# Kernel tuning notes

Hardware: AMD Instinct MI355X
Metric: run time of the kernel (lower is better)

The kernel has to match this reference:

```python
import jax, jax.numpy as jnp
import numpy as np

N = 8192
IN_CH = 256
OUT_CH = 256


def setup_inputs() -> dict:
    key = jax.random.key(0)
    k1, k2, k3, k4, k5 = jax.random.split(key, 5)
    features = jax.random.normal(k1, (N, IN_CH), dtype=jnp.float32)
    wavelets = jax.random.normal(k2, (N, N), dtype=jnp.float32)
    wavelets_inv = jax.random.normal(k3, (N, N), dtype=jnp.float32)
    # parameters
    # xavier uniform for weight_matrix
    limit = np.sqrt(6.0 / (IN_CH + OUT_CH)).astype(np.float32)
    weight_matrix = jax.random.uniform(k4, (IN_CH, OUT_CH), minval=-limit, maxval=limit, dtype=jnp.float32)
    filt = jax.random.uniform(k5, (N,), minval=0.9, maxval=1.1, dtype=jnp.float32)
    return {"features": features, "wavelets": wavelets, "wavelets_inv": wavelets_inv,
            "weight_matrix": weight_matrix, "filt": filt}


def reference(features, wavelets, wavelets_inv, weight_matrix, filt):
    # transformed = features @ W                    [N, out]
    transformed = features @ weight_matrix
    # spectral = wavelets_inv @ transformed         [N, out]
    spectral = wavelets_inv @ transformed
    # torch.diag(filter) @ spectral == filt[:, None] * spectral (avoid NxN diag GEMM)
    filtered = filt[:, None] * spectral
    # output = wavelets @ filtered                  [N, out]
    return wavelets @ filtered
```

## Files before the change

### kernel.cpp

```cpp
#include <hip/hip_runtime.h>
#include <hip/hip_bf16.h>
#include <stdint.h>
#include <stddef.h>

typedef __bf16 bf16;
typedef float f32x4 __attribute__((ext_vector_type(4)));
typedef bf16 bf16x8 __attribute__((ext_vector_type(8)));
typedef bf16 bf16x4 __attribute__((ext_vector_type(4)));

#define MROWS 8192
#define NOUT 256
#define BK 128
#define NTHREADS 512
#define LDS_SMALL (32 * BK * 2)

#define SCHED0 __builtin_amdgcn_sched_barrier(0)
#define SBAR __builtin_amdgcn_s_barrier()


__global__ __launch_bounds__(NTHREADS, 1) void gemm_ks(
    const float* __restrict__ A, const bf16* __restrict__ Bp,
    float* __restrict__ wsP, float* __restrict__ doutP,
    const int kshift, const int nsteps, const int lda) {
  __shared__ char lds[2][32768];
  const int t = threadIdx.x;
  const int w = t >> 6;
  const int l = t & 63;
  const int ks = blockIdx.x & ((1 << kshift) - 1);
  const int mt = blockIdx.x >> kshift;
  const int m0 = mt * 128;
  const int ts0 = ks * nsteps;
  float* __restrict__ Ps =
      (ks == ((1 << kshift) - 1)) ? doutP : wsP + (size_t)ks * 2097152;

  const float* gAr[4];
#pragma unroll
  for (int j = 0; j < 4; ++j)
    gAr[j] = A + (size_t)(m0 + w * 16 + j * 2 + (l >> 5)) * (size_t)lda +
             (size_t)ts0 * BK + (l & 31) * 4;

  int awoff[8];
#pragma unroll
  for (int q = 0; q < 8; ++q) {
    const int r = w * 16 + q * 2 + (l >> 5);
    awoff[q] = r * 256 + ((((l & 31) * 8)) ^ ((r & 7) << 4));
  }

  int aoffb[4];
#pragma unroll
  for (int ak = 0; ak < 4; ++ak)
    aoffb[ak] = (l & 15) * 256 +
                ((ak * 64 + (l >> 4) * 16) ^ ((l & 7) << 4));

  const char* pBw = (const char*)Bp + w * 8192 + l * 16;

  f32x4 acc[8][2] = {};
  f32x4 pA[8];
  bf16x8 Ba[2][4], Bb[2][4];

#define LOAD_PA(KA)                                                           \
  {                                                                           \
    _Pragma("unroll") for (int j = 0; j < 4; ++j) {                           \
      pA[2 * j] = __builtin_nontemporal_load((const f32x4*)(gAr[j] + (KA)));  \
      pA[2 * j + 1] = __builtin_nontemporal_load(                             \
          (const f32x4*)(gAr[j] + (size_t)2 * lda * 4 / 4 * 0 + 0) + 0);      \
    }                                                                         \
  }
#undef LOAD_PA
  const float* gAq[8];
#pragma unroll
  for (int q = 0; q < 8; ++q)
    gAq[q] = A + (size_t)(m0 + w * 16 + q * 2 + (l >> 5)) * (size_t)lda +
             (size_t)ts0 * BK + (l & 31) * 4;

#pragma unroll
  for (int q = 0; q < 8; ++q)
    pA[q] = __builtin_nontemporal_load((const f32x4*)gAq[q]);
  SCHED0;
#pragma unroll
  for (int bfi = 0; bfi < 2; ++bfi)
#pragma unroll
    for (int ak = 0; ak < 4; ++ak)
      Ba[bfi][ak] = *(const bf16x8*)(pBw + ((size_t)ts0 << 16) +
                                     (bfi * 4 + ak) * 1024);
  SCHED0;
#pragma unroll
  for (int q = 0; q < 8; ++q) {
    bf16x4 pk;
#pragma unroll
    for (int e = 0; e < 4; ++e) pk[e] = (bf16)pA[q][e];
    *(bf16x4*)(lds[0] + awoff[q]) = pk;
  }
  SCHED0;
  {
    const int s1 = (nsteps > 1) ? BK : 0;
#pragma unroll
    for (int q = 0; q < 8; ++q)
      pA[q] = __builtin_nontemporal_load((const f32x4*)(gAq[q] + s1));
  }
  asm volatile("s_waitcnt lgkmcnt(0)" ::: "memory");
  SBAR;
  SCHED0;

#define BODY_K(S, PAR, BCUR, BNXT)                                            \
  {                                                                           \
    const char* rslot = lds[PAR];                                             \
    char* wslot = lds[PAR ^ 1];                                               \
    _Pragma("unroll") for (int q = 0; q < 8; ++q) {                           \
      bf16x4 pk;                                                              \
      _Pragma("unroll") for (int e = 0; e < 4; ++e) pk[e] = (bf16)pA[q][e];   \
      *(bf16x4*)(wslot + awoff[q]) = pk;                                      \
    }                                                                         \
    SCHED0;                                                                   \
    {                                                                         \
      const int tn = ((S) + 1 < nsteps) ? ts0 + (S) + 1 : ts0;                \
      _Pragma("unroll") for (int bfi = 0; bfi < 2; ++bfi)                     \
          _Pragma("unroll") for (int ak = 0; ak < 4; ++ak)                    \
              BNXT[bfi][ak] = *(const bf16x8*)(                               \
                  pBw + ((size_t)tn << 16) + (bfi * 4 + ak) * 1024);          \
    }                                                                         \
    SCHED0;                                                                   \
    {                                                                         \
      const int ka = ((S) + 2 < nsteps) ? ((S) + 2) * BK : 0;                 \
      _Pragma("unroll") for (int q = 0; q < 8; ++q)                           \
          pA[q] = __builtin_nontemporal_load((const f32x4*)(gAq[q] + ka));    \
    }                                                                         \
    SCHED0;                                                                   \
    __builtin_amdgcn_s_setprio(1);                                            \
    _Pragma("unroll") for (int ak = 0; ak < 4; ++ak) {                        \
      bf16x8 afr[8];                                                          \
      _Pragma("unroll") for (int af = 0; af < 8; ++af)                        \
          afr[af] = *(const bf16x8*)(rslot + af * 4096 + aoffb[ak]);          \
      _Pragma("unroll") for (int af = 0; af < 8; ++af)                        \
          _Pragma("unroll") for (int bfi = 0; bfi < 2; ++bfi)                 \
              acc[af][bfi] = __builtin_amdgcn_mfma_f32_16x16x32_bf16(         \
                  afr[af], BCUR[bfi][ak], acc[af][bfi], 0, 0, 0);             \
    }                                                                         \
    __builtin_amdgcn_s_setprio(0);                                            \
    SCHED0;                                                                   \
    asm volatile("s_waitcnt lgkmcnt(0)" ::: "memory");                        \
    SBAR;                                                                     \
    SCHED0;                                                                   \
  }

  for (int s = 0; s < nsteps; s += 2) {
    BODY_K(s, 0, Ba, Bb);
    BODY_K(s + 1, 1, Bb, Ba);
  }
#undef BODY_K

#pragma unroll
  for (int af = 0; af < 8; ++af)
#pragma unroll
    for (int bfi = 0; bfi < 2; ++bfi) {
      const int mb = m0 + af * 16 + (l >> 4) * 4;
      const int n = w * 32 + bfi * 16 + (l & 15);
#pragma unroll
      for (int j = 0; j < 4; ++j)
        Ps[(size_t)(mb + j) * NOUT + n] = acc[af][bfi][j];
    }
}

__global__ void reduce2(const float* __restrict__ wsP,
                        const float* __restrict__ doutP,
                        const float* __restrict__ filt, bf16* __restrict__ Fp,
                        const int KS) {
  const int n = threadIdx.x;
  const int m8 = blockIdx.x;
  bf16x8 pk;
#pragma unroll
  for (int r = 0; r < 8; ++r) {
    const int m = m8 * 8 + r;
    float s = doutP[(size_t)m * NOUT + n];
    for (int ks = 0; ks < KS - 1; ++ks)
      s += wsP[(size_t)ks * 2097152 + (size_t)m * NOUT + n];
    pk[r] = (bf16)(s * filt[m]);
  }
  const int ts = m8 >> 4, wq = n >> 5, bq = (n >> 4) & 1, aq = (m8 >> 2) & 3;
  const int lq = (m8 & 3) * 16 + (n & 15);
  *(bf16x8*)((char*)Fp +
             (size_t)(((ts * 64 + wq * 8 + bq * 4 + aq) << 10) + lq * 16)) = pk;
}

__global__ void reduce3(const float* __restrict__ wsP, float* __restrict__ doutP,
                        const int KS) {
  const size_t i = (size_t)blockIdx.x * 256 + threadIdx.x;
  float s = doutP[i];
  for (int ks = 0; ks < KS - 1; ++ks) s += wsP[(size_t)ks * 2097152 + i];
  doutP[i] = s;
}

template <bool SCALE, bool OUTT>
__global__ __launch_bounds__(NTHREADS, 1) void gemm_small(
    const float* __restrict__ A, const bf16* __restrict__ Bp,
    const float* __restrict__ filt, void* __restrict__ outp,
    const int K, const int lda) {
  __shared__ char lds[2][LDS_SMALL];
  const int t = threadIdx.x;
  const int w = t >> 6;
  const int l = t & 63;
  const int m0 = blockIdx.x * 32;
  const int NT = K / BK;

  const int ar = t >> 4;
  const int acb = t & 15;
  const float* gA = A + (size_t)(m0 + ar) * (size_t)lda + acb * 8;
  const int a_lds_off = (ar * (BK * 2) + acb * 16) ^ ((ar & 7) << 4);

  int aoff[2][4];
#pragma unroll
  for (int af = 0; af < 2; ++af)
#pragma unroll
    for (int ak = 0; ak < 4; ++ak) {
      const int r = af * 16 + (l & 15);
      const int kb = ak * 64 + (l >> 4) * 16;
      aoff[af][ak] = (r * (BK * 2) + kb) ^ ((r & 7) << 4);
    }

  const char* pBw = (const char*)Bp + w * 8192 + l * 16;

  f32x4 acc[2][2] = {};

  f32x4 aS0a = __builtin_nontemporal_load((const f32x4*)gA);
  f32x4 aS0b = __builtin_nontemporal_load((const f32x4*)gA + 1);
  f32x4 aS1a = __builtin_nontemporal_load((const f32x4*)(gA + BK));
  f32x4 aS1b = __builtin_nontemporal_load((const f32x4*)(gA + BK) + 1);
  bf16x8 Bc[2][4], Bn[2][4];
#pragma unroll
  for (int bfi = 0; bfi < 2; ++bfi)
#pragma unroll
    for (int ak = 0; ak < 4; ++ak)
      Bc[bfi][ak] = *(const bf16x8*)(pBw + (bfi * 4 + ak) * 1024);
  {
    bf16x8 pk;
#pragma unroll
    for (int j = 0; j < 4; ++j) { pk[j] = (bf16)aS0a[j]; pk[j + 4] = (bf16)aS0b[j]; }
    *(bf16x8*)(lds[0] + a_lds_off) = pk;
  }
  asm volatile("s_waitcnt lgkmcnt(0)" ::: "memory");
  SBAR;
  SCHED0;

#define BODY_S(TS, P, BCUR, BNXT, AW0, AW1, AL0, AL1)                         \
  {                                                                           \
    const char* bb = lds[P];                                                  \
    bf16x8 afr[2][4];                                                         \
    _Pragma("unroll") for (int af = 0; af < 2; ++af)                          \
        _Pragma("unroll") for (int ak = 0; ak < 4; ++ak)                      \
            afr[af][ak] = *(const bf16x8*)(bb + aoff[af][ak]);                \
    SCHED0;                                                                   \
    const size_t kb1 = (size_t)((((TS) + 1) < NT ? ((TS) + 1) : 0)) << 16;    \
    _Pragma("unroll") for (int bfi = 0; bfi < 2; ++bfi)                       \
        _Pragma("unroll") for (int ak = 0; ak < 4; ++ak)                      \
            BNXT[bfi][ak] =                                                   \
                *(const bf16x8*)(pBw + kb1 + (bfi * 4 + ak) * 1024);          \
    SCHED0;                                                                   \
    const int ka2 = (((TS) + 2) < NT ? ((TS) + 2) : 0) * BK;                  \
    AL0 = __builtin_nontemporal_load((const f32x4*)(gA + ka2));               \
    AL1 = __builtin_nontemporal_load((const f32x4*)(gA + ka2) + 1);           \
    SCHED0;                                                                   \
    asm volatile("s_waitcnt lgkmcnt(0)" ::: "memory");                        \
    SCHED0;                                                                   \
    __builtin_amdgcn_s_setprio(1);                                            \
    _Pragma("unroll") for (int ak = 0; ak < 4; ++ak)                          \
        _Pragma("unroll") for (int af = 0; af < 2; ++af)                      \
            _Pragma("unroll") for (int bfi = 0; bfi < 2; ++bfi)               \
                acc[af][bfi] = __builtin_amdgcn_mfma_f32_16x16x32_bf16(       \
                    afr[af][ak], BCUR[bfi][ak], acc[af][bfi], 0, 0, 0);       \
    __builtin_amdgcn_s_setprio(0);                                            \
    SCHED0;                                                                   \
    {                                                                         \
      bf16x8 pk;                                                              \
      _Pragma("unroll") for (int j = 0; j < 4; ++j) {                         \
        pk[j] = (bf16)AW0[j];                                                 \
        pk[j + 4] = (bf16)AW1[j];                                             \
      }                                                                       \
      *(bf16x8*)(lds[P ^ 1] + a_lds_off) = pk;                                \
    }                                                                         \
    asm volatile("s_waitcnt lgkmcnt(0)" ::: "memory");                        \
    SBAR;                                                                     \
    SCHED0;                                                                   \
  }

  for (int ts = 0; ts < NT; ts += 2) {
    BODY_S(ts, 0, Bc, Bn, aS1a, aS1b, aS0a, aS0b);
    BODY_S(ts + 1, 1, Bn, Bc, aS0a, aS0b, aS1a, aS1b);
  }
#undef BODY_S

#pragma unroll
  for (int af = 0; af < 2; ++af)
#pragma unroll
    for (int bfi = 0; bfi < 2; ++bfi) {
      const int mb = m0 + af * 16 + (l >> 4) * 4;
      const int n = w * 32 + bfi * 16 + (l & 15);
      f32x4 v = acc[af][bfi];
      if (SCALE) {
#pragma unroll
        for (int j = 0; j < 4; ++j) v[j] *= filt[mb + j];
      }
      if (OUTT) {
        bf16x4 pv;
#pragma unroll
        for (int j = 0; j < 4; ++j) pv[j] = (bf16)v[j];
        const int tsq = mb >> 7, wq = n >> 5, bq = (n >> 4) & 1, aq = (mb >> 5) & 3;
        const int lq = ((mb >> 3) & 3) * 16 + (n & 15);
        char* dst = (char*)outp +
                    (size_t)(((tsq * 64 + wq * 8 + bq * 4 + aq) << 10) + lq * 16 +
                             (mb & 7) * 2);
        *(bf16x4*)dst = pv;
      } else {
        float* po = (float*)outp + (size_t)mb * NOUT + n;
#pragma unroll
        for (int j = 0; j < 4; ++j) po[(size_t)j * NOUT] = v[j];
      }
    }
}

__global__ void prep_wt(const float* __restrict__ W, bf16* __restrict__ Wp) {
  const int k = blockIdx.x;
  const int n = threadIdx.x;
  const int off = (((k >> 7) * 64 + (n >> 5) * 8 + ((n >> 4) & 1) * 4 +
                    ((k >> 5) & 3)) << 10) +
                  (((k >> 3) & 3) * 16 + (n & 15)) * 16 + (k & 7) * 2;
  *(bf16*)((char*)Wp + off) = (bf16)W[k * 256 + n];
}

extern "C" void kernel_launch(void* const* d_in, const int* in_sizes, int n_in,
                              void* d_out, int out_size, void* d_ws, size_t ws_size,
                              hipStream_t stream) {
  const float* features = (const float*)d_in[0];
  const float* wavelets = (const float*)d_in[1];
  const float* wavelets_inv = (const float*)d_in[2];
  const float* W = (const float*)d_in[3];
  const float* filt = (const float*)d_in[4];
  float* out = (float*)d_out;

  char* ws = (char*)d_ws;
  bf16* Wp = (bf16*)ws;
  bf16* Tp = (bf16*)(ws + 131072);
  bf16* Fp = (bf16*)(ws + 131072 + 4194304);
  float* wsP = (float*)(ws + 131072 + 8388608);

  const size_t base = 131072 + 8388608;
  int KS = 0, kshift = 0;
  if (ws_size >= base + 3u * 8388608u) { KS = 4; kshift = 2; }
  else if (ws_size >= base + 1u * 8388608u) { KS = 2; kshift = 1; }

  prep_wt<<<256, 256, 0, stream>>>(W, Wp);
  gemm_small<false, true><<<256, NTHREADS, 0, stream>>>(features, Wp, nullptr, Tp, 256, 256);

  if (KS) {
    const int nsteps = 64 / KS;
    gemm_ks<<<64 * KS, NTHREADS, 0, stream>>>(wavelets_inv, Tp, wsP, out, kshift, nsteps, 8192);
    reduce2<<<1024, 256, 0, stream>>>(wsP, out, filt, Fp, KS);
    gemm_ks<<<64 * KS, NTHREADS, 0, stream>>>(wavelets, Fp, wsP, out, kshift, nsteps, 8192);
    reduce3<<<8192, 256, 0, stream>>>(wsP, out, KS);
  } else {
    gemm_ks<<<64, NTHREADS, 0, stream>>>(wavelets_inv, Tp, wsP, out, 0, 64, 8192);
    reduce2<<<1024, 256, 0, stream>>>(wsP, out, filt, Fp, 1);
    gemm_ks<<<64, NTHREADS, 0, stream>>>(wavelets, Fp, wsP, out, 0, 64, 8192);
  }
}
```

Baseline: 160.2 us.

## Stage A in 256-wide K panels with one barrier per two MFMA substeps

Restructures the split-K GEMM main loop so each LDS stage holds a 128x256 A panel, loaded row-per-wavefront in two halves of 8 rows. The panel is consumed as two 128-wide K substeps with interleaved B register prefetch, which halves the number of block barriers per K. The cost is doubled LDS usage (128 KB), a new swizzle layout, and an implicit assumption that nsteps is even.

```diff
diff --git a/kernel.cpp b/kernel.cpp
--- a/kernel.cpp
+++ b/kernel.cpp
@@ -22,7 +22,7 @@
     const float* __restrict__ A, const bf16* __restrict__ Bp,
     float* __restrict__ wsP, float* __restrict__ doutP,
     const int kshift, const int nsteps, const int lda) {
-  __shared__ char lds[2][32768];
+  __shared__ char lds[2][65536];
   const int t = threadIdx.x;
   const int w = t >> 6;
   const int l = t & 63;
@@ -30,27 +30,29 @@
   const int mt = blockIdx.x >> kshift;
   const int m0 = mt * 128;
   const int ts0 = ks * nsteps;
+  const int npan = nsteps >> 1;
   float* __restrict__ Ps =
       (ks == ((1 << kshift) - 1)) ? doutP : wsP + (size_t)ks * 2097152;
 
-  const float* gAr[4];
-#pragma unroll
-  for (int j = 0; j < 4; ++j)
-    gAr[j] = A + (size_t)(m0 + w * 16 + j * 2 + (l >> 5)) * (size_t)lda +
-             (size_t)ts0 * BK + (l & 31) * 4;
+  const float* gAq[8];
+#pragma unroll
+  for (int q = 0; q < 8; ++q)
+    gAq[q] = A + (size_t)(m0 + w * 16 + q) * (size_t)lda +
+             (size_t)ts0 * BK + l * 4;
+  const size_t row8 = (size_t)8 * (size_t)lda;
 
   int awoff[8];
 #pragma unroll
-  for (int q = 0; q < 8; ++q) {
-    const int r = w * 16 + q * 2 + (l >> 5);
-    awoff[q] = r * 256 + ((((l & 31) * 8)) ^ ((r & 7) << 4));
-  }
-
-  int aoffb[4];
-#pragma unroll
-  for (int ak = 0; ak < 4; ++ak)
-    aoffb[ak] = (l & 15) * 256 +
-                ((ak * 64 + (l >> 4) * 16) ^ ((l & 7) << 4));
+  for (int q = 0; q < 8; ++q)
+    awoff[q] = (w * 16 + q) * 512 + ((l * 8) ^ (q << 4));
+
+  int aoffb[2][4];
+#pragma unroll
+  for (int ss = 0; ss < 2; ++ss)
+#pragma unroll
+    for (int ak = 0; ak < 4; ++ak)
+      aoffb[ss][ak] = (l & 15) * 512 +
+                      ((ss * 256 + ak * 64 + (l >> 4) * 16) ^ ((l & 7) << 4));
 
   const char* pBw = (const char*)Bp + w * 8192 + l * 16;
 
@@ -58,96 +60,88 @@
   f32x4 pA[8];
   bf16x8 Ba[2][4], Bb[2][4];
 
-#define LOAD_PA(KA)                                                           \
-  {                                                                           \
-    _Pragma("unroll") for (int j = 0; j < 4; ++j) {                           \
-      pA[2 * j] = __builtin_nontemporal_load((const f32x4*)(gAr[j] + (KA)));  \
-      pA[2 * j + 1] = __builtin_nontemporal_load(                             \
-          (const f32x4*)(gAr[j] + (size_t)2 * lda * 4 / 4 * 0 + 0) + 0);      \
-    }                                                                         \
-  }
-#undef LOAD_PA
-  const float* gAq[8];
-#pragma unroll
-  for (int q = 0; q < 8; ++q)
-    gAq[q] = A + (size_t)(m0 + w * 16 + q * 2 + (l >> 5)) * (size_t)lda +
-             (size_t)ts0 * BK + (l & 31) * 4;
-
-#pragma unroll
-  for (int q = 0; q < 8; ++q)
-    pA[q] = __builtin_nontemporal_load((const f32x4*)gAq[q]);
-  SCHED0;
-#pragma unroll
-  for (int bfi = 0; bfi < 2; ++bfi)
-#pragma unroll
-    for (int ak = 0; ak < 4; ++ak)
-      Ba[bfi][ak] = *(const bf16x8*)(pBw + ((size_t)ts0 << 16) +
-                                     (bfi * 4 + ak) * 1024);
-  SCHED0;
-#pragma unroll
-  for (int q = 0; q < 8; ++q) {
-    bf16x4 pk;
-#pragma unroll
-    for (int e = 0; e < 4; ++e) pk[e] = (bf16)pA[q][e];
-    *(bf16x4*)(lds[0] + awoff[q]) = pk;
-  }
-  SCHED0;
-  {
-    const int s1 = (nsteps > 1) ? BK : 0;
-#pragma unroll
-    for (int q = 0; q < 8; ++q)
-      pA[q] = __builtin_nontemporal_load((const f32x4*)(gAq[q] + s1));
-  }
-  asm volatile("s_waitcnt lgkmcnt(0)" ::: "memory");
-  SBAR;
-  SCHED0;
-
-#define BODY_K(S, PAR, BCUR, BNXT)                                            \
-  {                                                                           \
-    const char* rslot = lds[PAR];                                             \
-    char* wslot = lds[PAR ^ 1];                                               \
+#define LOADA_P(PP)                                                           \
+  {                                                                           \
+    const int ko = (((PP) < npan) ? (PP) : 0) * 256;                          \
+    _Pragma("unroll") for (int q = 0; q < 8; ++q)                             \
+        pA[q] = __builtin_nontemporal_load((const f32x4*)(gAq[q] + ko));      \
+  }
+#define LOADB_P(PP)                                                           \
+  {                                                                           \
+    const int ko = (((PP) < npan) ? (PP) : 0) * 256;                          \
+    _Pragma("unroll") for (int q = 0; q < 8; ++q)                             \
+        pA[q] = __builtin_nontemporal_load(                                   \
+            (const f32x4*)(gAq[q] + row8 + ko));                              \
+  }
+#define WRITE_P(SLOT, EXTRA)                                                  \
+  {                                                                           \
     _Pragma("unroll") for (int q = 0; q < 8; ++q) {                           \
       bf16x4 pk;                                                              \
       _Pragma("unroll") for (int e = 0; e < 4; ++e) pk[e] = (bf16)pA[q][e];   \
-      *(bf16x4*)(wslot + awoff[q]) = pk;                                      \
+      *(bf16x4*)((SLOT) + awoff[q] + (EXTRA)) = pk;                           \
     }                                                                         \
-    SCHED0;                                                                   \
-    {                                                                         \
-      const int tn = ((S) + 1 < nsteps) ? ts0 + (S) + 1 : ts0;                \
-      _Pragma("unroll") for (int bfi = 0; bfi < 2; ++bfi)                     \
-          _Pragma("unroll") for (int ak = 0; ak < 4; ++ak)                    \
-              BNXT[bfi][ak] = *(const bf16x8*)(                               \
-                  pBw + ((size_t)tn << 16) + (bfi * 4 + ak) * 1024);          \
-    }                                                                         \
-    SCHED0;                                                                   \
-    {                                                                         \
-      const int ka = ((S) + 2 < nsteps) ? ((S) + 2) * BK : 0;                 \
-      _Pragma("unroll") for (int q = 0; q < 8; ++q)                           \
-          pA[q] = __builtin_nontemporal_load((const f32x4*)(gAq[q] + ka));    \
-    }                                                                         \
-    SCHED0;                                                                   \
+  }
+#define LOADB_REGS(TSX, DST)                                                  \
+  {                                                                           \
+    const int tn = (((TSX) < nsteps) ? ts0 + (TSX) : ts0);                    \
+    _Pragma("unroll") for (int bfi = 0; bfi < 2; ++bfi)                       \
+        _Pragma("unroll") for (int ak = 0; ak < 4; ++ak)                      \
+            DST[bfi][ak] = *(const bf16x8*)(                                  \
+                pBw + ((size_t)tn << 16) + (bfi * 4 + ak) * 1024);            \
+  }
+#define MFMA_SS(SS, BSET, RSLOT)                                              \
+  {                                                                           \
     __builtin_amdgcn_s_setprio(1);                                            \
     _Pragma("unroll") for (int ak = 0; ak < 4; ++ak) {                        \
       bf16x8 afr[8];                                                          \
       _Pragma("unroll") for (int af = 0; af < 8; ++af)                        \
-          afr[af] = *(const bf16x8*)(rslot + af * 4096 + aoffb[ak]);          \
+          afr[af] = *(const bf16x8*)((RSLOT) + af * 8192 + aoffb[SS][ak]);    \
       _Pragma("unroll") for (int af = 0; af < 8; ++af)                        \
           _Pragma("unroll") for (int bfi = 0; bfi < 2; ++bfi)                 \
               acc[af][bfi] = __builtin_amdgcn_mfma_f32_16x16x32_bf16(         \
-                  afr[af], BCUR[bfi][ak], acc[af][bfi], 0, 0, 0);             \
+                  afr[af], BSET[bfi][ak], acc[af][bfi], 0, 0, 0);             \
     }                                                                         \
     __builtin_amdgcn_s_setprio(0);                                            \
-    SCHED0;                                                                   \
-    asm volatile("s_waitcnt lgkmcnt(0)" ::: "memory");                        \
-    SBAR;                                                                     \
-    SCHED0;                                                                   \
-  }
-
-  for (int s = 0; s < nsteps; s += 2) {
-    BODY_K(s, 0, Ba, Bb);
-    BODY_K(s + 1, 1, Bb, Ba);
-  }
-#undef BODY_K
+  }
+
+  LOADA_P(0);
+  WRITE_P(lds[0], 0);
+  LOADB_P(0);
+  WRITE_P(lds[0], 4096);
+  LOADB_REGS(0, Ba);
+  LOADA_P(1);
+  asm volatile("s_waitcnt lgkmcnt(0)" ::: "memory");
+  SBAR;
+  SCHED0;
+
+  for (int p = 0; p < npan; ++p) {
+    const char* rslot = lds[p & 1];
+    char* wslot = lds[(p & 1) ^ 1];
+    WRITE_P(wslot, 0);
+    SCHED0;
+    LOADB_P(p + 1);
+    SCHED0;
+    LOADB_REGS(2 * p + 1, Bb);
+    SCHED0;
+    MFMA_SS(0, Ba, rslot);
+    SCHED0;
+    WRITE_P(wslot, 4096);
+    SCHED0;
+    LOADA_P(p + 2);
+    SCHED0;
+    LOADB_REGS(2 * p + 2, Ba);
+    SCHED0;
+    MFMA_SS(1, Bb, rslot);
+    SCHED0;
+    asm volatile("s_waitcnt lgkmcnt(0)" ::: "memory");
+    SBAR;
+    SCHED0;
+  }
+#undef LOADA_P
+#undef LOADB_P
+#undef WRITE_P
+#undef LOADB_REGS
+#undef MFMA_SS
 
 #pragma unroll
   for (int af = 0; af < 8; ++af)
```

After: 170.0 us. +6.1%, slower.
